# Kernel optimization log

Hardware: AMD Instinct MI355X
Metric: run time of the kernel (lower is better)

Reference implementation:

```python
import jax, jax.numpy as jnp
import numpy as np
from jax import lax

# 4th-order Butterworth lowpass, scipy.signal.butter(4, 0.2)
B_COEF = np.array([0.004824343357716228, 0.019297373430864913, 0.02894606014629737,
                   0.019297373430864913, 0.004824343357716228], dtype=np.float32)
A_COEF = np.array([1.0, -2.369513007182038, 2.3139884144006453,
                   -1.0546654058785672, 0.18737949236818502], dtype=np.float32)


def setup_inputs() -> dict:
    key = jax.random.key(0)
    x = jax.random.normal(key, (8, 64, 48000), dtype=jnp.float32)
    return {"x": x, "b": jnp.asarray(B_COEF), "a": jnp.asarray(A_COEF)}


def _pad_odd(x, n):
    # Faithful to torch _pad_odd (including its exact slicing on the right side).
    left = 2.0 * x[..., 0:1] - jnp.flip(x[..., 0:n], axis=-1)
    right = 2.0 * x[..., -1:] - jnp.flip(x[..., -(n + 2):-2], axis=-1)
    return jnp.concatenate([left, x, right], axis=-1)


def _lfilter(x, a, b):
    # y[n] = (sum_k b[k] x[n-k] - sum_j a[j] y[n-j]) / a[0]
    a0 = a[0]
    bn = b / a0
    an = a[1:] / a0                      # [N], N = order
    ntaps = b.shape[0]                   # static
    N = a.shape[0] - 1                   # static
    T = x.shape[-1]
    # FIR part: small static tap loop, fully vectorized over batch/time.
    pad = [(0, 0)] * (x.ndim - 1) + [(ntaps - 1, 0)]
    xp = jnp.pad(x, pad)
    f = bn[0] * xp[..., ntaps - 1: ntaps - 1 + T]
    for k in range(1, ntaps):
        f = f + bn[k] * xp[..., ntaps - 1 - k: ntaps - 1 - k + T]
    # IIR recurrence via scan over time.
    f_t = jnp.moveaxis(f, -1, 0)         # [T, B, C]
    init = jnp.zeros(x.shape[:-1] + (N,), x.dtype)  # [B, C, N], y[t-1..t-N]

    def step(carry, ft):
        y = ft - jnp.einsum('k,...k->...', an, carry)
        carry = jnp.concatenate([y[..., None], carry[..., :-1]], axis=-1)
        return carry, y

    _, ys = lax.scan(step, init, f_t)
    return jnp.moveaxis(ys, 0, -1)       # [B, C, T]


def _filtfilt(x, a, b):
    y = _lfilter(x, a, b)
    return jnp.flip(_lfilter(jnp.flip(y, axis=-1), a, b), axis=-1)


def reference(x, b, a):
    scale = jnp.max(jnp.abs(x), axis=-1, keepdims=True)
    xs = x / scale
    padlen = 3 * max(int(a.shape[0]), int(b.shape[0]))  # 15, static
    xp = _pad_odd(xs, padlen)
    y = _filtfilt(xp, a, b)
    y = y[..., padlen:-padlen]
    return y * scale
```

## Files before the change

### kernel.cpp

```cpp
#include <hip/hip_runtime.h>


#define T48 48000
#define TP0 48030
#define LCH 48
#define NOUT 251

#define BAR_LDS() do { \
  asm volatile("s_waitcnt lgkmcnt(0)" ::: "memory"); \
  __builtin_amdgcn_s_barrier(); \
} while (0)

__device__ __forceinline__ float fget(const float4& v, int e) {
  switch (e & 3) { case 0: return v.x; case 1: return v.y; case 2: return v.z; default: return v.w; }
}

#define MAPPLY(t, M, q) do { \
  (t).x += (M)[0]*(q).x  + (M)[1]*(q).y  + (M)[2]*(q).z  + (M)[3]*(q).w; \
  (t).y += (M)[4]*(q).x  + (M)[5]*(q).y  + (M)[6]*(q).z  + (M)[7]*(q).w; \
  (t).z += (M)[8]*(q).x  + (M)[9]*(q).y  + (M)[10]*(q).z + (M)[11]*(q).w; \
  (t).w += (M)[12]*(q).x + (M)[13]*(q).y + (M)[14]*(q).z + (M)[15]*(q).w; \
} while (0)

__global__ __launch_bounds__(256, 4) void filtfilt_k(
    const float* __restrict__ x, const float* __restrict__ bco,
    const float* __restrict__ aco, float* __restrict__ out)
{
  __shared__ __align__(16) float4 S[1024];
  __shared__ float P0s[16];

  const int t   = threadIdx.x;
  const int seq = blockIdx.x >> 2;
  const int b   = blockIdx.x & 3;
  const int gc  = NOUT*b - 2 + t;
  const float* __restrict__ xs = x + (size_t)seq * T48;
  const float4* __restrict__ xs4 = reinterpret_cast<const float4*>(xs);
  float* __restrict__ os = out + (size_t)seq * T48;
  float4* __restrict__ os4 = reinterpret_cast<float4*>(os);

  const float inva0 = 1.f / aco[0];
  const float b0 = bco[0]*inva0, b1 = bco[1]*inva0, b2 = bco[2]*inva0,
              b3 = bco[3]*inva0, b4 = bco[4]*inva0;
  const float na1 = -aco[1]*inva0, na2 = -aco[2]*inva0,
              na3 = -aco[3]*inva0, na4 = -aco[4]*inva0;

  float4 F[14];
  const int fb = 12*gc - 5;
#pragma unroll
  for (int k = 0; k < 14; k++) {
    int m = min(max(fb + k, 0), 11999);
    F[k] = xs4[m];
  }

  if (t < 64) {
    const int i = (t >> 2) & 3, j = t & 3;
    float r1 = (j==0)?1.f:0.f, r2 = (j==1)?1.f:0.f,
          r3 = (j==2)?1.f:0.f, r4 = (j==3)?1.f:0.f;
#pragma unroll
    for (int n = 0; n < LCH; n++) {
      float h = fmaf(na1, r1, fmaf(na2, r2, fmaf(na3, r3, na4 * r4)));
      r4 = r3; r3 = r2; r2 = r1; r1 = h;
    }
    float c0 = __shfl(r1, j), c1 = __shfl(r2, j),
          c2 = __shfl(r3, j), c3 = __shfl(r4, j);
    float Pv = (i==0)?c0 : (i==1)?c1 : (i==2)?c2 : c3;
    if (t < 16) P0s[t] = Pv;
  }

  float w4v = F[0].y, w3v = F[0].z, w2v = F[0].w, w1v = F[1].x;
  float A[LCH];
#pragma unroll
  for (int n = 0; n < LCH; n++) A[n] = fget(F[(n + 5) >> 2], (n + 5) & 3);

  if (gc < 0) {
    w4v = 0.f; w3v = 0.f; w2v = 0.f; w1v = 0.f;
#pragma unroll
    for (int n = 0; n < LCH; n++) A[n] = 0.f;
  } else if (gc == 0) {
    float x0d = 2.f * xs[0];
    w4v = 0.f; w3v = 0.f; w2v = 0.f; w1v = 0.f;
#pragma unroll
    for (int n = 0; n < 15; n++) A[n] = x0d - xs[14 - n];
  }
  if (gc >= 1000) {
    float xld = 2.f * xs[T48 - 1];
#define RFIX(p, var) do { int _p = (p); \
    if (_p >= 48015) var = (_p < TP0) ? (xld - xs[96012 - _p]) : 0.f; } while (0)
    RFIX(48*gc - 4, w4v); RFIX(48*gc - 3, w3v);
    RFIX(48*gc - 2, w2v); RFIX(48*gc - 1, w1v);
#pragma unroll
    for (int n = 0; n < LCH; n++) {
      int p = 48*gc + n;
      if (p >= 48015) A[n] = (p < TP0) ? (xld - xs[96012 - p]) : 0.f;
    }
#undef RFIX
  }

  float r1 = 0.f, r2 = 0.f, r3 = 0.f, r4 = 0.f;
#pragma unroll
  for (int n = 0; n < LCH; n++) {
    float xv = A[n];
    float f = fmaf(b0,xv, fmaf(b1,w1v, fmaf(b2,w2v, fmaf(b3,w3v, b4*w4v))));
    w4v = w3v; w3v = w2v; w2v = w1v; w1v = xv;
    float u = fmaf(na4, r4, f);
    u = fmaf(na3, r3, u); u = fmaf(na2, r2, u); u = fmaf(na1, r1, u);
    A[n] = u; r4 = r3; r3 = r2; r2 = r1; r1 = u;
  }

  S[t] = make_float4(r1, r2, r3, r4);
  BAR_LDS();
  float4 sv = make_float4(0.f,0.f,0.f,0.f);
  if (t >= 2) {
    sv = S[t-1];
    float4 q = S[t-2];
    MAPPLY(sv, P0s, q);
  }

  {
    float h1 = sv.x, h2 = sv.y, h3 = sv.z, h4 = sv.w;
#pragma unroll
    for (int n = 0; n < LCH; n++) {
      float h = fmaf(na1, h1, fmaf(na2, h2, fmaf(na3, h3, na4 * h4)));
      A[n] += h;
      h4 = h3; h3 = h2; h2 = h1; h1 = h;
    }
  }
  if (gc >= 1000) {
#pragma unroll
    for (int n = 0; n < LCH; n++) if (48*gc + n >= TP0) A[n] = 0.f;
  }

  S[256 + t] = make_float4(A[0], A[1], A[2], A[3]);
  BAR_LDS();
  float h0 = 0.f, h1v = 0.f, h2v = 0.f, h3v = 0.f;
  if (t < 255) { float4 hv = S[256 + t + 1]; h0 = hv.x; h1v = hv.y; h2v = hv.z; h3v = hv.w; }

#define YV(i) ((i) < 48 ? A[(i)] : ((i)==48 ? h0 : (i)==49 ? h1v : (i)==50 ? h2v : h3v))
  r1 = 0.f; r2 = 0.f; r3 = 0.f; r4 = 0.f;
#pragma unroll
  for (int m = 0; m < LCH; m++) {
    float g = fmaf(b0, YV(47-m), fmaf(b1, YV(48-m),
              fmaf(b2, YV(49-m), fmaf(b3, YV(50-m), b4 * YV(51-m)))));
    float u = fmaf(na4, r4, g);
    u = fmaf(na3, r3, u); u = fmaf(na2, r2, u); u = fmaf(na1, r1, u);
    r4 = r3; r3 = r2; r2 = r1; r1 = u;
    if      (m == 0) h3v = u;
    else if (m == 1) h2v = u;
    else if (m == 2) h1v = u;
    else if (m == 3) h0  = u;
    else             A[51 - m] = u;
  }
#undef YV

  S[512 + t] = make_float4(r1, r2, r3, r4);
  BAR_LDS();
  float4 ev = make_float4(0.f,0.f,0.f,0.f);
  if (t < 255) {
    ev = S[512 + t + 1];
    if (t < 254) { float4 q = S[512 + t + 2]; MAPPLY(ev, P0s, q); }
  }
  BAR_LDS();

  {
    float g1 = ev.x, g2 = ev.y, g3 = ev.z, g4 = ev.w;
#pragma unroll
    for (int m = 0; m < LCH; m++) {
      float h = fmaf(na1, g1, fmaf(na2, g2, fmaf(na3, g3, na4 * g4)));
      if      (m == 0) h3v += h;
      else if (m == 1) h2v += h;
      else if (m == 2) h1v += h;
      else if (m == 3) h0  += h;
      else             A[51 - m] += h;
      g4 = g3; g3 = g2; g2 = g1; g1 = h;
    }
  }

  S[4*t + 0] = make_float4(A[4],  A[5],  A[6],  A[7]);
  S[4*t + 1] = make_float4(A[8],  A[9],  A[10], A[11]);
  S[4*t + 2] = make_float4(A[12], A[13], A[14], A[15]);
  S[4*t + 3] = make_float4(A[16], A[17], A[18], A[19]);
  BAR_LDS();
  if (t >= 2 && t < 253 && gc <= 999) {
    float4 N0 = S[4*t + 4], N1 = S[4*t + 5], N2 = S[4*t + 6], N3 = S[4*t + 7];
    float4* op = os4 + 12*gc;
#pragma unroll
    for (int k = 0; k < 7; k++)
      op[k] = make_float4(A[19+4*k], A[20+4*k], A[21+4*k], A[22+4*k]);
    op[7]  = make_float4(A[47], h0, h1v, h2v);
    op[8]  = make_float4(h3v, N0.x, N0.y, N0.z);
    op[9]  = make_float4(N0.w, N1.x, N1.y, N1.z);
    op[10] = make_float4(N1.w, N2.x, N2.y, N2.z);
    op[11] = make_float4(N2.w, N3.x, N3.y, N3.z);
  }
}

extern "C" void kernel_launch(void* const* d_in, const int* in_sizes, int n_in,
                              void* d_out, int out_size, void* d_ws, size_t ws_size,
                              hipStream_t stream) {
  (void)n_in; (void)d_ws; (void)ws_size; (void)out_size;
  const float* x = (const float*)d_in[0];
  const float* b = (const float*)d_in[1];
  const float* a = (const float*)d_in[2];
  float* out = (float*)d_out;
  const int nseq = in_sizes[0] / T48;
  filtfilt_k<<<dim3(nseq * 4), dim3(256), 0, stream>>>(x, b, a, out);
}
```

Before: 199.1 us.

## Halve per-thread chunk length to 24 with 512-thread blocks and 4-chunk state propagation

Each thread now processes 24 samples instead of 48, and blocks grow from 256 to 512 threads, so each block still covers roughly 2000 samples. Halving the chunk means the 48-step impulse decay is no longer enough for a neighbour-only correction, so the carry fix-up now uses four preceding chunks, with matrix powers P, P^2 and P^3 precomputed through shuffles. This cuts the serial recurrence length per thread and the register footprint of A and F, which should allow better latency hiding. The cost is more halo work, more LDS traffic in the matrix correction, and a larger LDS footprint per block.

Measured after the change: 202.7 us. Within noise of the previous version (+1.8%).

```diff
diff --git a/kernel.cpp b/kernel.cpp
--- a/kernel.cpp
+++ b/kernel.cpp
@@ -3,8 +3,8 @@
 
 #define T48 48000
 #define TP0 48030
-#define LCH 48
-#define NOUT 251
+#define LCH 24
+#define UPB 504
 
 #define BAR_LDS() do { \
   asm volatile("s_waitcnt lgkmcnt(0)" ::: "memory"); \
@@ -22,17 +22,17 @@
   (t).w += (M)[12]*(q).x + (M)[13]*(q).y + (M)[14]*(q).z + (M)[15]*(q).w; \
 } while (0)
 
-__global__ __launch_bounds__(256, 4) void filtfilt_k(
+__global__ __launch_bounds__(512, 4) void filtfilt_k(
     const float* __restrict__ x, const float* __restrict__ bco,
     const float* __restrict__ aco, float* __restrict__ out)
 {
-  __shared__ __align__(16) float4 S[1024];
-  __shared__ float P0s[16];
+  __shared__ __align__(16) float4 S[2048];
+  __shared__ float P[3][16];
 
   const int t   = threadIdx.x;
   const int seq = blockIdx.x >> 2;
   const int b   = blockIdx.x & 3;
-  const int gc  = NOUT*b - 2 + t;
+  const int gc  = UPB*b - 4 + t;
   const float* __restrict__ xs = x + (size_t)seq * T48;
   const float4* __restrict__ xs4 = reinterpret_cast<const float4*>(xs);
   float* __restrict__ os = out + (size_t)seq * T48;
@@ -44,10 +44,10 @@
   const float na1 = -aco[1]*inva0, na2 = -aco[2]*inva0,
               na3 = -aco[3]*inva0, na4 = -aco[4]*inva0;
 
-  float4 F[14];
-  const int fb = 12*gc - 5;
-#pragma unroll
-  for (int k = 0; k < 14; k++) {
+  float4 F[8];
+  const int fb = 6*gc - 5;
+#pragma unroll
+  for (int k = 0; k < 8; k++) {
     int m = min(max(fb + k, 0), 11999);
     F[k] = xs4[m];
   }
@@ -64,7 +64,24 @@
     float c0 = __shfl(r1, j), c1 = __shfl(r2, j),
           c2 = __shfl(r3, j), c3 = __shfl(r4, j);
     float Pv = (i==0)?c0 : (i==1)?c1 : (i==2)?c2 : c3;
-    if (t < 16) P0s[t] = Pv;
+    if (t < 16) P[0][t] = Pv;
+    const float P0v = Pv;
+    {
+      float rA0 = __shfl(Pv, i*4+0), rA1 = __shfl(Pv, i*4+1),
+            rA2 = __shfl(Pv, i*4+2), rA3 = __shfl(Pv, i*4+3);
+      float cB0 = __shfl(Pv, 0*4+j), cB1 = __shfl(Pv, 1*4+j),
+            cB2 = __shfl(Pv, 2*4+j), cB3 = __shfl(Pv, 3*4+j);
+      Pv = rA0*cB0 + rA1*cB1 + rA2*cB2 + rA3*cB3;
+    }
+    if (t < 16) P[1][t] = Pv;
+    {
+      float rA0 = __shfl(Pv, i*4+0), rA1 = __shfl(Pv, i*4+1),
+            rA2 = __shfl(Pv, i*4+2), rA3 = __shfl(Pv, i*4+3);
+      float cB0 = __shfl(P0v, 0*4+j), cB1 = __shfl(P0v, 1*4+j),
+            cB2 = __shfl(P0v, 2*4+j), cB3 = __shfl(P0v, 3*4+j);
+      Pv = rA0*cB0 + rA1*cB1 + rA2*cB2 + rA3*cB3;
+    }
+    if (t < 16) P[2][t] = Pv;
   }
 
   float w4v = F[0].y, w3v = F[0].z, w2v = F[0].w, w1v = F[1].x;
@@ -82,15 +99,15 @@
 #pragma unroll
     for (int n = 0; n < 15; n++) A[n] = x0d - xs[14 - n];
   }
-  if (gc >= 1000) {
+  if (gc >= 2000) {
     float xld = 2.f * xs[T48 - 1];
 #define RFIX(p, var) do { int _p = (p); \
     if (_p >= 48015) var = (_p < TP0) ? (xld - xs[96012 - _p]) : 0.f; } while (0)
-    RFIX(48*gc - 4, w4v); RFIX(48*gc - 3, w3v);
-    RFIX(48*gc - 2, w2v); RFIX(48*gc - 1, w1v);
+    RFIX(24*gc - 4, w4v); RFIX(24*gc - 3, w3v);
+    RFIX(24*gc - 2, w2v); RFIX(24*gc - 1, w1v);
 #pragma unroll
     for (int n = 0; n < LCH; n++) {
-      int p = 48*gc + n;
+      int p = 24*gc + n;
       if (p >= 48015) A[n] = (p < TP0) ? (xld - xs[96012 - p]) : 0.f;
     }
 #undef RFIX
@@ -110,11 +127,10 @@
   S[t] = make_float4(r1, r2, r3, r4);
   BAR_LDS();
   float4 sv = make_float4(0.f,0.f,0.f,0.f);
-  if (t >= 2) {
-    sv = S[t-1];
-    float4 q = S[t-2];
-    MAPPLY(sv, P0s, q);
-  }
+  if (t >= 1) sv = S[t-1];
+  if (t >= 2) { float4 q = S[t-2]; MAPPLY(sv, P[0], q); }
+  if (t >= 3) { float4 q = S[t-3]; MAPPLY(sv, P[1], q); }
+  if (t >= 4) { float4 q = S[t-4]; MAPPLY(sv, P[2], q); }
 
   {
     float h1 = sv.x, h2 = sv.y, h3 = sv.z, h4 = sv.w;
@@ -125,22 +141,22 @@
       h4 = h3; h3 = h2; h2 = h1; h1 = h;
     }
   }
-  if (gc >= 1000) {
-#pragma unroll
-    for (int n = 0; n < LCH; n++) if (48*gc + n >= TP0) A[n] = 0.f;
-  }
-
-  S[256 + t] = make_float4(A[0], A[1], A[2], A[3]);
+  if (gc >= 2000) {
+#pragma unroll
+    for (int n = 0; n < LCH; n++) if (24*gc + n >= TP0) A[n] = 0.f;
+  }
+
+  S[512 + t] = make_float4(A[0], A[1], A[2], A[3]);
   BAR_LDS();
   float h0 = 0.f, h1v = 0.f, h2v = 0.f, h3v = 0.f;
-  if (t < 255) { float4 hv = S[256 + t + 1]; h0 = hv.x; h1v = hv.y; h2v = hv.z; h3v = hv.w; }
-
-#define YV(i) ((i) < 48 ? A[(i)] : ((i)==48 ? h0 : (i)==49 ? h1v : (i)==50 ? h2v : h3v))
+  if (t < 511) { float4 hv = S[512 + t + 1]; h0 = hv.x; h1v = hv.y; h2v = hv.z; h3v = hv.w; }
+
+#define YV(i) ((i) < 24 ? A[(i)] : ((i)==24 ? h0 : (i)==25 ? h1v : (i)==26 ? h2v : h3v))
   r1 = 0.f; r2 = 0.f; r3 = 0.f; r4 = 0.f;
 #pragma unroll
   for (int m = 0; m < LCH; m++) {
-    float g = fmaf(b0, YV(47-m), fmaf(b1, YV(48-m),
-              fmaf(b2, YV(49-m), fmaf(b3, YV(50-m), b4 * YV(51-m)))));
+    float g = fmaf(b0, YV(23-m), fmaf(b1, YV(24-m),
+              fmaf(b2, YV(25-m), fmaf(b3, YV(26-m), b4 * YV(27-m)))));
     float u = fmaf(na4, r4, g);
     u = fmaf(na3, r3, u); u = fmaf(na2, r2, u); u = fmaf(na1, r1, u);
     r4 = r3; r3 = r2; r2 = r1; r1 = u;
@@ -148,17 +164,17 @@
     else if (m == 1) h2v = u;
     else if (m == 2) h1v = u;
     else if (m == 3) h0  = u;
-    else             A[51 - m] = u;
+    else             A[27 - m] = u;
   }
 #undef YV
 
-  S[512 + t] = make_float4(r1, r2, r3, r4);
+  S[1024 + t] = make_float4(r1, r2, r3, r4);
   BAR_LDS();
   float4 ev = make_float4(0.f,0.f,0.f,0.f);
-  if (t < 255) {
-    ev = S[512 + t + 1];
-    if (t < 254) { float4 q = S[512 + t + 2]; MAPPLY(ev, P0s, q); }
-  }
+  if (t <= 510) ev = S[1024 + t + 1];
+  if (t <= 509) { float4 q = S[1024 + t + 2]; MAPPLY(ev, P[0], q); }
+  if (t <= 508) { float4 q = S[1024 + t + 3]; MAPPLY(ev, P[1], q); }
+  if (t <= 507) { float4 q = S[1024 + t + 4]; MAPPLY(ev, P[2], q); }
   BAR_LDS();
 
   {
@@ -170,27 +186,25 @@
       else if (m == 1) h2v += h;
       else if (m == 2) h1v += h;
       else if (m == 3) h0  += h;
-      else             A[51 - m] += h;
+      else             A[27 - m] += h;
       g4 = g3; g3 = g2; g2 = g1; g1 = h;
     }
   }
 
-  S[4*t + 0] = make_float4(A[4],  A[5],  A[6],  A[7]);
-  S[4*t + 1] = make_float4(A[8],  A[9],  A[10], A[11]);
-  S[4*t + 2] = make_float4(A[12], A[13], A[14], A[15]);
-  S[4*t + 3] = make_float4(A[16], A[17], A[18], A[19]);
-  BAR_LDS();
-  if (t >= 2 && t < 253 && gc <= 999) {
-    float4 N0 = S[4*t + 4], N1 = S[4*t + 5], N2 = S[4*t + 6], N3 = S[4*t + 7];
-    float4* op = os4 + 12*gc;
-#pragma unroll
-    for (int k = 0; k < 7; k++)
-      op[k] = make_float4(A[19+4*k], A[20+4*k], A[21+4*k], A[22+4*k]);
-    op[7]  = make_float4(A[47], h0, h1v, h2v);
-    op[8]  = make_float4(h3v, N0.x, N0.y, N0.z);
-    op[9]  = make_float4(N0.w, N1.x, N1.y, N1.z);
-    op[10] = make_float4(N1.w, N2.x, N2.y, N2.z);
-    op[11] = make_float4(N2.w, N3.x, N3.y, N3.z);
+  S[t]        = make_float4(A[4],  A[5],  A[6],  A[7]);
+  S[512 + t]  = make_float4(A[8],  A[9],  A[10], A[11]);
+  S[1024 + t] = make_float4(A[12], A[13], A[14], A[15]);
+  S[1536 + t] = make_float4(A[16], A[17], A[18], A[19]);
+  BAR_LDS();
+  if (t >= 4 && t < 508 && gc <= 1999) {
+    float4 N0 = S[t+1], N1 = S[512 + t+1], N2 = S[1024 + t+1], N3 = S[1536 + t+1];
+    float4* op = os4 + 6*gc;
+    op[0] = make_float4(A[19], A[20], A[21], A[22]);
+    op[1] = make_float4(A[23], h0,    h1v,   h2v);
+    op[2] = make_float4(h3v,   N0.x,  N0.y,  N0.z);
+    op[3] = make_float4(N0.w,  N1.x,  N1.y,  N1.z);
+    op[4] = make_float4(N1.w,  N2.x,  N2.y,  N2.z);
+    op[5] = make_float4(N2.w,  N3.x,  N3.y,  N3.z);
   }
 }
 
@@ -203,5 +217,5 @@
   const float* a = (const float*)d_in[2];
   float* out = (float*)d_out;
   const int nseq = in_sizes[0] / T48;
-  filtfilt_k<<<dim3(nseq * 4), dim3(256), 0, stream>>>(x, b, a, out);
+  filtfilt_k<<<dim3(nseq * 4), dim3(512), 0, stream>>>(x, b, a, out);
 }
```
